# Optimization experiments

Hardware: AMD Instinct MI355X
Metric: run time of the kernel (lower is better)

## Reference

```python
import jax, jax.numpy as jnp
import numpy as np


def _neighbor_indices(e):
    """Replicates the Python branch ladder: for each position i pick two key/value
    slice indices (k1, k2) based on entropy comparisons with neighbors."""
    S = e.shape[0]
    i = jnp.arange(S)
    e_prev = e[jnp.clip(i - 1, 0, S - 1)]
    e_next = e[jnp.clip(i + 1, 0, S - 1)]
    ge_next = e >= e_next
    ge_prev = e >= e_prev
    le_next = e <= e_next
    le_prev = e <= e_prev
    # branch order matters for ties: check in the same order as the torch code
    c1 = ge_next & ge_prev  # local max  -> (i-1, i+1)
    c2 = le_next & ge_prev  # rising     -> (i-1, i)
    c3 = ge_next & le_prev  # falling    -> (i,   i+1)
    k1 = jnp.where(c1, i - 1, jnp.where(c2, i - 1, jnp.where(c3, i, i)))
    k2 = jnp.where(c1, i + 1, jnp.where(c2, i, jnp.where(c3, i + 1, i)))
    # boundary i == 0: (1,1) if e0 >= e1 else (0,0)
    b0 = jnp.where(e[0] >= e[1], 1, 0)
    k1 = k1.at[0].set(b0)
    k2 = k2.at[0].set(b0)
    # boundary i == S-1: (S-2,S-2) if e[-1] >= e[-2] else (S-1,S-1)
    bL = jnp.where(e[S - 1] >= e[S - 2], S - 2, S - 1)
    k1 = k1.at[S - 1].set(bL)
    k2 = k2.at[S - 1].set(bL)
    return k1, k2


def setup_inputs() -> dict:
    key = jax.random.key(0)
    k1, k2 = jax.random.split(key)
    S, C, H, W = 64, 512, 32, 32
    c5d = jax.random.normal(k1, (S, C, H, W), dtype=jnp.float32)
    entropy_list = jax.random.uniform(k2, (S,), dtype=jnp.float32)
    return {"c5d": c5d, "entropy_list": entropy_list}


def reference(c5d, entropy_list):
    S = c5d.shape[0]
    D = int(np.prod(c5d.shape[1:]))
    k1, k2 = _neighbor_indices(entropy_list)
    idx = jnp.stack([k1, k2], axis=1)              # [S, 2]
    q = c5d.reshape(S, D)                          # [S, D]  one token per slice
    kv = q[idx]                                    # [S, 2, D] gathered neighbor tokens
    scale = 1.0 / jnp.sqrt(jnp.asarray(D, dtype=q.dtype))
    scores = jnp.einsum("sd,skd->sk", q, kv) * scale   # [S, 2]
    attn = jax.nn.softmax(scores, axis=-1)
    out = jnp.einsum("sk,skd->sd", attn, kv)           # [S, D]
    return out.reshape(c5d.shape)
```

## Files before the change

kernel.cpp:

```cpp
#include <hip/hip_runtime.h>
#include <math.h>

#define NSLICE 64
#define DVEC   131072
#define NB     32
#define CHUNK4 (DVEC/NB)
#define TPB    256

__inline__ __device__ float wave_reduce(float v) {
    #pragma unroll
    for (int off = 32; off > 0; off >>= 1) v += __shfl_down(v, off, 64);
    return v;
}

__global__ __launch_bounds__(TPB) void dots_kernel(
        const float* __restrict__ q, float* __restrict__ norms, float* __restrict__ adj) {
    const int i = blockIdx.y;
    const int j = blockIdx.x;
    const bool has_next = (i < NSLICE - 1);
    const float4* qi = (const float4*)q + (size_t)i * DVEC + (size_t)j * CHUNK4;
    const float4* qn = qi + DVEC;

    float self = 0.f, cross = 0.f;
    for (int t = threadIdx.x; t < CHUNK4; t += TPB) {
        float4 a = qi[t];
        self += a.x*a.x + a.y*a.y + a.z*a.z + a.w*a.w;
        if (has_next) {
            float4 b = qn[t];
            cross += a.x*b.x + a.y*b.y + a.z*b.z + a.w*b.w;
        }
    }

    __shared__ float s_s[TPB / 64];
    __shared__ float s_c[TPB / 64];
    float sw = wave_reduce(self);
    float cw = wave_reduce(cross);
    const int lane = threadIdx.x & 63;
    const int wid  = threadIdx.x >> 6;
    if (lane == 0) { s_s[wid] = sw; s_c[wid] = cw; }
    __syncthreads();
    if (threadIdx.x == 0) {
        float st = s_s[0] + s_s[1] + s_s[2] + s_s[3];
        float ct = s_c[0] + s_c[1] + s_c[2] + s_c[3];
        atomicAdd(&norms[i], st);
        if (has_next) atomicAdd(&adj[i], ct);
    }
}

__global__ void weights_kernel(
        const float* __restrict__ e, const float* __restrict__ norms,
        const float* __restrict__ adj, float* __restrict__ w1o, float* __restrict__ w2o,
        int* __restrict__ ao, int* __restrict__ bo) {
    const int i = threadIdx.x;
    const float ei = e[i];
    int k1, k2;
    if (i == 0) {
        const int b0 = (ei >= e[1]) ? 1 : 0;
        k1 = b0; k2 = b0;
    } else if (i == NSLICE - 1) {
        const int bL = (ei >= e[NSLICE - 2]) ? (NSLICE - 2) : (NSLICE - 1);
        k1 = bL; k2 = bL;
    } else {
        const float ep = e[i - 1], en = e[i + 1];
        const bool ge_next = (ei >= en), ge_prev = (ei >= ep);
        const bool le_next = (ei <= en), le_prev = (ei <= ep);
        if      (ge_next && ge_prev) { k1 = i - 1; k2 = i + 1; }
        else if (le_next && ge_prev) { k1 = i - 1; k2 = i;     }
        else if (ge_next && le_prev) { k1 = i;     k2 = i + 1; }
        else                         { k1 = i;     k2 = i;     }
    }
    const float di  = norms[i];
    const float dlo = (i > 0) ? adj[i - 1] : 0.f;
    const float dhi = (i < NSLICE - 1) ? adj[i] : 0.f;
    const float s_scale = 1.0f / sqrtf(524288.0f);
    const float s1 = ((k1 < i) ? dlo : (k1 > i) ? dhi : di) * s_scale;
    const float s2 = ((k2 < i) ? dlo : (k2 > i) ? dhi : di) * s_scale;
    const float m  = fmaxf(s1, s2);
    const float e1 = expf(s1 - m), e2 = expf(s2 - m);
    const float inv = 1.0f / (e1 + e2);
    w1o[i] = e1 * inv;
    w2o[i] = e2 * inv;
    ao[i] = k1;
    bo[i] = k2;
}

__global__ __launch_bounds__(TPB) void combine_kernel(
        const float* __restrict__ q, const float* __restrict__ w1,
        const float* __restrict__ w2, const int* __restrict__ ai,
        const int* __restrict__ bi, float* __restrict__ out) {
    const int i = blockIdx.y;
    const int j = blockIdx.x;
    const float wa = w1[i];
    const float wb = w2[i];
    const int a = ai[i];
    const int b = bi[i];
    const float4* qa = (const float4*)q + (size_t)a * DVEC + (size_t)j * CHUNK4;
    const float4* qb = (const float4*)q + (size_t)b * DVEC + (size_t)j * CHUNK4;
    float4* o = (float4*)out + (size_t)i * DVEC + (size_t)j * CHUNK4;
    for (int t = threadIdx.x; t < CHUNK4; t += TPB) {
        float4 x = qa[t];
        float4 y = qb[t];
        float4 r;
        r.x = wa * x.x + wb * y.x;
        r.y = wa * x.y + wb * y.y;
        r.z = wa * x.z + wb * y.z;
        r.w = wa * x.w + wb * y.w;
        o[t] = r;
    }
}

extern "C" void kernel_launch(void* const* d_in, const int* in_sizes, int n_in,
                              void* d_out, int out_size, void* d_ws, size_t ws_size,
                              hipStream_t stream) {
    const float* c5d = (const float*)d_in[0];
    const float* ent = (const float*)d_in[1];
    float* out = (float*)d_out;

    float* norms = (float*)d_ws;
    float* adj   = norms + NSLICE;
    float* w1    = adj + NSLICE;
    float* w2    = w1 + NSLICE;
    int*   a     = (int*)(w2 + NSLICE);
    int*   b     = a + NSLICE;

    hipMemsetAsync(d_ws, 0, 2 * NSLICE * sizeof(float), stream);

    dots_kernel<<<dim3(NB, NSLICE), TPB, 0, stream>>>(c5d, norms, adj);
    weights_kernel<<<1, NSLICE, 0, stream>>>(ent, norms, adj, w1, w2, a, b);
    combine_kernel<<<dim3(NB, NSLICE), TPB, 0, stream>>>(c5d, w1, w2, a, b, out);
}
```

Before: 257.4 us.

## Fuse dot, weight and combine kernels into one cooperative persistent kernel

Replaces the memset and three kernel launches with a single cooperative kernel of 1024 blocks. Each block first writes per-chunk partial norms and neighbour dots, then a grid-wide sync separates that phase from the combine phase. In the combine phase each block recomputes the softmax weights by summing its 32 partials, which removes the atomics, the memset and the tiny single-block weights kernel. The costs are a grid barrier, redundant small reductions per task, and reliance on a cooperative launch with all 1024 blocks co-resident.

```diff
diff --git a/kernel.cpp b/kernel.cpp
--- a/kernel.cpp
+++ b/kernel.cpp
@@ -1,11 +1,16 @@
 #include <hip/hip_runtime.h>
+#include <hip/hip_cooperative_groups.h>
 #include <math.h>
+
+namespace cg = cooperative_groups;
 
 #define NSLICE 64
 #define DVEC   131072
 #define NB     32
-#define CHUNK4 (DVEC/NB)
+#define CHUNK4 (DVEC / NB)
 #define TPB    256
+#define NBLK   1024
+#define NTASK  (NSLICE * NB)
 
 __inline__ __device__ float wave_reduce(float v) {
     #pragma unroll
@@ -13,99 +18,102 @@
     return v;
 }
 
-__global__ __launch_bounds__(TPB) void dots_kernel(
-        const float* __restrict__ q, float* __restrict__ norms, float* __restrict__ adj) {
-    const int i = blockIdx.y;
-    const int j = blockIdx.x;
-    const bool has_next = (i < NSLICE - 1);
-    const float4* qi = (const float4*)q + (size_t)i * DVEC + (size_t)j * CHUNK4;
-    const float4* qn = qi + DVEC;
+__global__ __launch_bounds__(TPB, 4) void fused_kernel(
+        const float* __restrict__ q, const float* __restrict__ ent,
+        float* __restrict__ pS, float* __restrict__ pC,
+        float* __restrict__ out) {
+    cg::grid_group grid = cg::this_grid();
+    __shared__ float s_s[TPB / 64];
+    __shared__ float s_c[TPB / 64];
 
-    float self = 0.f, cross = 0.f;
-    for (int t = threadIdx.x; t < CHUNK4; t += TPB) {
-        float4 a = qi[t];
-        self += a.x*a.x + a.y*a.y + a.z*a.z + a.w*a.w;
-        if (has_next) {
-            float4 b = qn[t];
-            cross += a.x*b.x + a.y*b.y + a.z*b.z + a.w*b.w;
+    for (int task = blockIdx.x; task < NTASK; task += NBLK) {
+        const int i = task >> 5;
+        const int j = task & 31;
+        const bool has_next = (i < NSLICE - 1);
+        const float4* qi = (const float4*)q + (size_t)i * DVEC + (size_t)j * CHUNK4;
+        const float4* qn = qi + DVEC;
+
+        float self = 0.f, cross = 0.f;
+        for (int t = threadIdx.x; t < CHUNK4; t += TPB) {
+            float4 a = qi[t];
+            self += a.x*a.x + a.y*a.y + a.z*a.z + a.w*a.w;
+            if (has_next) {
+                float4 b = qn[t];
+                cross += a.x*b.x + a.y*b.y + a.z*b.z + a.w*b.w;
+            }
         }
+        const float sw = wave_reduce(self);
+        const float cw = wave_reduce(cross);
+        const int lane = threadIdx.x & 63;
+        const int wid  = threadIdx.x >> 6;
+        if (lane == 0) { s_s[wid] = sw; s_c[wid] = cw; }
+        __syncthreads();
+        if (threadIdx.x == 0) {
+            pS[task] = s_s[0] + s_s[1] + s_s[2] + s_s[3];
+            pC[task] = s_c[0] + s_c[1] + s_c[2] + s_c[3];
+        }
+        __syncthreads();
     }
 
-    __shared__ float s_s[TPB / 64];
-    __shared__ float s_c[TPB / 64];
-    float sw = wave_reduce(self);
-    float cw = wave_reduce(cross);
-    const int lane = threadIdx.x & 63;
-    const int wid  = threadIdx.x >> 6;
-    if (lane == 0) { s_s[wid] = sw; s_c[wid] = cw; }
-    __syncthreads();
-    if (threadIdx.x == 0) {
-        float st = s_s[0] + s_s[1] + s_s[2] + s_s[3];
-        float ct = s_c[0] + s_c[1] + s_c[2] + s_c[3];
-        atomicAdd(&norms[i], st);
-        if (has_next) atomicAdd(&adj[i], ct);
-    }
-}
+    __threadfence();
+    grid.sync();
 
-__global__ void weights_kernel(
-        const float* __restrict__ e, const float* __restrict__ norms,
-        const float* __restrict__ adj, float* __restrict__ w1o, float* __restrict__ w2o,
-        int* __restrict__ ao, int* __restrict__ bo) {
-    const int i = threadIdx.x;
-    const float ei = e[i];
-    int k1, k2;
-    if (i == 0) {
-        const int b0 = (ei >= e[1]) ? 1 : 0;
-        k1 = b0; k2 = b0;
-    } else if (i == NSLICE - 1) {
-        const int bL = (ei >= e[NSLICE - 2]) ? (NSLICE - 2) : (NSLICE - 1);
-        k1 = bL; k2 = bL;
-    } else {
-        const float ep = e[i - 1], en = e[i + 1];
-        const bool ge_next = (ei >= en), ge_prev = (ei >= ep);
-        const bool le_next = (ei <= en), le_prev = (ei <= ep);
-        if      (ge_next && ge_prev) { k1 = i - 1; k2 = i + 1; }
-        else if (le_next && ge_prev) { k1 = i - 1; k2 = i;     }
-        else if (ge_next && le_prev) { k1 = i;     k2 = i + 1; }
-        else                         { k1 = i;     k2 = i;     }
-    }
-    const float di  = norms[i];
-    const float dlo = (i > 0) ? adj[i - 1] : 0.f;
-    const float dhi = (i < NSLICE - 1) ? adj[i] : 0.f;
-    const float s_scale = 1.0f / sqrtf(524288.0f);
-    const float s1 = ((k1 < i) ? dlo : (k1 > i) ? dhi : di) * s_scale;
-    const float s2 = ((k2 < i) ? dlo : (k2 > i) ? dhi : di) * s_scale;
-    const float m  = fmaxf(s1, s2);
-    const float e1 = expf(s1 - m), e2 = expf(s2 - m);
-    const float inv = 1.0f / (e1 + e2);
-    w1o[i] = e1 * inv;
-    w2o[i] = e2 * inv;
-    ao[i] = k1;
-    bo[i] = k2;
-}
+    for (int task = blockIdx.x; task < NTASK; task += NBLK) {
+        const int i = task >> 5;
+        const int j = task & 31;
 
-__global__ __launch_bounds__(TPB) void combine_kernel(
-        const float* __restrict__ q, const float* __restrict__ w1,
-        const float* __restrict__ w2, const int* __restrict__ ai,
-        const int* __restrict__ bi, float* __restrict__ out) {
-    const int i = blockIdx.y;
-    const int j = blockIdx.x;
-    const float wa = w1[i];
-    const float wb = w2[i];
-    const int a = ai[i];
-    const int b = bi[i];
-    const float4* qa = (const float4*)q + (size_t)a * DVEC + (size_t)j * CHUNK4;
-    const float4* qb = (const float4*)q + (size_t)b * DVEC + (size_t)j * CHUNK4;
-    float4* o = (float4*)out + (size_t)i * DVEC + (size_t)j * CHUNK4;
-    for (int t = threadIdx.x; t < CHUNK4; t += TPB) {
-        float4 x = qa[t];
-        float4 y = qb[t];
-        float4 r;
-        r.x = wa * x.x + wb * y.x;
-        r.y = wa * x.y + wb * y.y;
-        r.z = wa * x.z + wb * y.z;
-        r.w = wa * x.w + wb * y.w;
-        o[t] = r;
+        float ni = 0.f, alo = 0.f, ahi = 0.f;
+        #pragma unroll 8
+        for (int t = 0; t < NB; t++) ni += pS[i * NB + t];
+        if (i > 0) {
+            #pragma unroll 8
+            for (int t = 0; t < NB; t++) alo += pC[(i - 1) * NB + t];
+        }
+        if (i < NSLICE - 1) {
+            #pragma unroll 8
+            for (int t = 0; t < NB; t++) ahi += pC[i * NB + t];
+        }
+
+        const float ei = ent[i];
+        int k1, k2;
+        if (i == 0) {
+            const int b0 = (ei >= ent[1]) ? 1 : 0;
+            k1 = b0; k2 = b0;
+        } else if (i == NSLICE - 1) {
+            const int bL = (ei >= ent[NSLICE - 2]) ? (NSLICE - 2) : (NSLICE - 1);
+            k1 = bL; k2 = bL;
+        } else {
+            const float ep = ent[i - 1], en = ent[i + 1];
+            const bool ge_next = (ei >= en), ge_prev = (ei >= ep);
+            const bool le_next = (ei <= en), le_prev = (ei <= ep);
+            if      (ge_next && ge_prev) { k1 = i - 1; k2 = i + 1; }
+            else if (le_next && ge_prev) { k1 = i - 1; k2 = i;     }
+            else if (ge_next && le_prev) { k1 = i;     k2 = i + 1; }
+            else                         { k1 = i;     k2 = i;     }
+        }
+
+        const float s_scale = 1.0f / sqrtf(524288.0f);
+        const float s1 = ((k1 < i) ? alo : (k1 > i) ? ahi : ni) * s_scale;
+        const float s2 = ((k2 < i) ? alo : (k2 > i) ? ahi : ni) * s_scale;
+        const float m  = fmaxf(s1, s2);
+        const float e1 = expf(s1 - m), e2 = expf(s2 - m);
+        const float inv = 1.0f / (e1 + e2);
+        const float wa = e1 * inv;
+        const float wb = e2 * inv;
+
+        const float4* qa = (const float4*)q + (size_t)k1 * DVEC + (size_t)j * CHUNK4;
+        const float4* qb = (const float4*)q + (size_t)k2 * DVEC + (size_t)j * CHUNK4;
+        float4* o = (float4*)out + (size_t)i * DVEC + (size_t)j * CHUNK4;
+        for (int t = threadIdx.x; t < CHUNK4; t += TPB) {
+            float4 x = qa[t];
+            float4 y = qb[t];
+            float4 r;
+            r.x = wa * x.x + wb * y.x;
+            r.y = wa * x.y + wb * y.y;
+            r.z = wa * x.z + wb * y.z;
+            r.w = wa * x.w + wb * y.w;
+            o[t] = r;
+        }
     }
 }
 
@@ -116,16 +124,10 @@
     const float* ent = (const float*)d_in[1];
     float* out = (float*)d_out;
 
-    float* norms = (float*)d_ws;
-    float* adj   = norms + NSLICE;
-    float* w1    = adj + NSLICE;
-    float* w2    = w1 + NSLICE;
-    int*   a     = (int*)(w2 + NSLICE);
-    int*   b     = a + NSLICE;
+    float* pS = (float*)d_ws;
+    float* pC = pS + NTASK;
 
-    hipMemsetAsync(d_ws, 0, 2 * NSLICE * sizeof(float), stream);
-
-    dots_kernel<<<dim3(NB, NSLICE), TPB, 0, stream>>>(c5d, norms, adj);
-    weights_kernel<<<1, NSLICE, 0, stream>>>(ent, norms, adj, w1, w2, a, b);
-    combine_kernel<<<dim3(NB, NSLICE), TPB, 0, stream>>>(c5d, w1, w2, a, b, out);
+    void* args[] = {(void*)&c5d, (void*)&ent, (void*)&pS, (void*)&pC, (void*)&out};
+    hipLaunchCooperativeKernel((void*)fused_kernel, dim3(NBLK), dim3(TPB),
+                               args, 0, stream);
 }
```

After: 391.5 us. +52.1%, slower.
